# Kernel tuning notes

Measured on AMD Instinct MI355X. Metric: run time of the kernel, lower is better.

The kernel has to match this reference:

```python
import jax, jax.numpy as jnp
import numpy as np

B, H, W, C = 8, 64, 64, 256
NB = 1000  # nms_topn proposals per image


def setup_inputs() -> dict:
    key = jax.random.key(0)
    k1, k2 = jax.random.split(key)
    fm = jax.random.normal(k1, (B, H, W, C), dtype=jnp.float32)
    # normalized boxes [y1,x1,y2,x2] with y1<=y2, x1<=x2
    pts = jax.random.uniform(k2, (B, NB, 2, 2), dtype=jnp.float32)
    pts = jnp.sort(pts, axis=2)  # [B,NB,2(min/max),2(y,x)]
    boxes = jnp.stack([pts[..., 0, 0], pts[..., 0, 1], pts[..., 1, 0], pts[..., 1, 1]], axis=-1)
    return {"feature_map": fm, "roi_bboxes": boxes, "pool_size": 7}


def _crop_and_resize(fm, boxes, box_idx, P):
    """Faithful TF tf.image.crop_and_resize (bilinear, extrapolation_value=0).
    fm: [B,H,W,C]; boxes: [N,4] normalized [y1,x1,y2,x2]; box_idx: [N] int.
    Returns [N,P,P,C]."""
    h, w = fm.shape[1], fm.shape[2]
    y1, x1, y2, x2 = boxes[:, 0], boxes[:, 1], boxes[:, 2], boxes[:, 3]
    t = jnp.arange(P, dtype=fm.dtype)
    # TF sampling grid for crop_size > 1: endpoints inclusive in pixel space
    ys = y1[:, None] * (h - 1) + t * ((y2 - y1)[:, None] * (h - 1) / (P - 1))  # [N,P]
    xs = x1[:, None] * (w - 1) + t * ((x2 - x1)[:, None] * (w - 1) / (P - 1))  # [N,P]

    def lin(coords, size):
        lo = jnp.floor(coords)
        frac = coords - lo
        lo_i = jnp.clip(lo, 0, size - 1).astype(jnp.int32)
        hi_i = jnp.clip(lo + 1, 0, size - 1).astype(jnp.int32)
        valid = (coords >= 0) & (coords <= size - 1)
        return lo_i, hi_i, frac, valid

    y_lo, y_hi, wy, vy = lin(ys, h)
    x_lo, x_hi, wx, vx = lin(xs, w)

    b = box_idx[:, None, None]
    v00 = fm[b, y_lo[:, :, None], x_lo[:, None, :]]  # [N,P,P,C]
    v01 = fm[b, y_lo[:, :, None], x_hi[:, None, :]]
    v10 = fm[b, y_hi[:, :, None], x_lo[:, None, :]]
    v11 = fm[b, y_hi[:, :, None], x_hi[:, None, :]]

    wy_ = wy[:, :, None, None]
    wx_ = wx[:, None, :, None]
    top = v00 + (v01 - v00) * wx_
    bot = v10 + (v11 - v10) * wx_
    out = top + (bot - top) * wy_

    valid = (vy[:, :, None] & vx[:, None, :])[..., None]
    return jnp.where(valid, out, jnp.zeros((), dtype=fm.dtype))


def reference(feature_map, roi_bboxes, pool_size):
    bs, nb = roi_bboxes.shape[0], roi_bboxes.shape[1]
    boxes = roi_bboxes.reshape(bs * nb, 4)
    box_idx = jnp.repeat(jnp.arange(bs, dtype=jnp.int32), nb)
    out = _crop_and_resize(feature_map, boxes, box_idx, pool_size)
    return out.reshape(bs, nb, pool_size, pool_size, feature_map.shape[-1])
```

## Files before the change

### kernel.cpp

```cpp
#include <hip/hip_runtime.h>


#define BATCH 8
#define FH 64
#define FW 64
#define FC 256
#define NBOX 1000
#define PP 7
#define POS_PER_BATCH (NBOX * PP * PP)
#define ROWS_PER_BATCH (NBOX * PP)

typedef __attribute__((ext_vector_type(4))) float f32x4;

__global__ __launch_bounds__(256, 3) void roi_align_kernel(
    const float* __restrict__ fm,
    const float* __restrict__ boxes,
    float* __restrict__ out)
{
    const int lane = threadIdx.x & 63;
    const int wib  = threadIdx.x >> 6;

    const int b    = blockIdx.x & 7;
    const int lblk = blockIdx.x >> 3;
    const int row  = lblk * 4 + wib;

    const int n  = row / PP;
    const int py = row % PP;

    const int c4 = lane * 4;
    const float* __restrict__ fmb = fm + (size_t)b * FH * FW * FC + c4;

    const float* bx = boxes + (b * NBOX + n) * 4;
    const float y1 = bx[0];
    const float x1 = bx[1];
    const float y2 = bx[2];
    const float x2 = bx[3];

    const float yc = y1 * (float)(FH - 1)
                   + (float)py * ((y2 - y1) * (float)(FH - 1) / (float)(PP - 1));
    const float ylo_f = floorf(yc);
    const float wy    = yc - ylo_f;
    int y_lo = (int)ylo_f;
    int y_hi = y_lo + 1;
    y_lo = min(max(y_lo, 0), FH - 1);
    y_hi = min(max(y_hi, 0), FH - 1);
    const bool vy = (yc >= 0.0f) && (yc <= (float)(FH - 1));

    const float xstep = (x2 - x1) * (float)(FW - 1) / (float)(PP - 1);
    const float xbase = x1 * (float)(FW - 1);

    const float* rlo = fmb + (size_t)(y_lo * FW) * FC;
    const float* rhi = fmb + (size_t)(y_hi * FW) * FC;

    float wxv[PP], vmask[PP];
    float4 v00[PP], v01[PP], v10[PP], v11[PP];

    #pragma unroll
    for (int px = 0; px < PP; ++px) {
        const float xc = xbase + (float)px * xstep;
        const float xlo_f = floorf(xc);
        wxv[px] = xc - xlo_f;
        int x_lo = (int)xlo_f;
        int x_hi = x_lo + 1;
        x_lo = min(max(x_lo, 0), FW - 1);
        x_hi = min(max(x_hi, 0), FW - 1);
        const bool vx = (xc >= 0.0f) && (xc <= (float)(FW - 1));
        vmask[px] = (vy && vx) ? 1.0f : 0.0f;

        v00[px] = *(const float4*)(rlo + (size_t)x_lo * FC);
        v01[px] = *(const float4*)(rlo + (size_t)x_hi * FC);
        v10[px] = *(const float4*)(rhi + (size_t)x_lo * FC);
        v11[px] = *(const float4*)(rhi + (size_t)x_hi * FC);
    }

    float* po = out + ((size_t)b * POS_PER_BATCH + (size_t)row * PP) * FC + c4;
    #pragma unroll
    for (int px = 0; px < PP; ++px) {
        const float wx = wxv[px], vm = vmask[px];
        float4 top, bot;
        f32x4 r;
        top.x = v00[px].x + (v01[px].x - v00[px].x) * wx;
        top.y = v00[px].y + (v01[px].y - v00[px].y) * wx;
        top.z = v00[px].z + (v01[px].z - v00[px].z) * wx;
        top.w = v00[px].w + (v01[px].w - v00[px].w) * wx;
        bot.x = v10[px].x + (v11[px].x - v10[px].x) * wx;
        bot.y = v10[px].y + (v11[px].y - v10[px].y) * wx;
        bot.z = v10[px].z + (v11[px].z - v10[px].z) * wx;
        bot.w = v10[px].w + (v11[px].w - v10[px].w) * wx;
        r.x = (top.x + (bot.x - top.x) * wy) * vm;
        r.y = (top.y + (bot.y - top.y) * wy) * vm;
        r.z = (top.z + (bot.z - top.z) * wy) * vm;
        r.w = (top.w + (bot.w - top.w) * wy) * vm;

        __builtin_nontemporal_store(r, (f32x4*)(po + (size_t)px * FC));
    }
}

extern "C" void kernel_launch(void* const* d_in, const int* in_sizes, int n_in,
                              void* d_out, int out_size, void* d_ws, size_t ws_size,
                              hipStream_t stream) {
    const float* fm    = (const float*)d_in[0];
    const float* boxes = (const float*)d_in[1];
    float* out = (float*)d_out;

    const int threads = 256;
    const int blocks  = BATCH * (ROWS_PER_BATCH / 4);

    roi_align_kernel<<<blocks, threads, 0, stream>>>(fm, boxes, out);
}
```

Measured before the change: 81.78 us.

## Convert feature map to bf16 in workspace before bilinear gather

Adds a pre-pass kernel that converts the fp32 feature map to bf16 in the workspace. The ROI-align kernel then gathers bf16 corners, halving gather bytes, and does the interpolation in fp32. The cost is an extra full read and write of the feature map each call, plus rounding error in the output. An fp32 fallback remains for when the workspace is too small.

```diff
diff --git a/kernel.cpp b/kernel.cpp
--- a/kernel.cpp
+++ b/kernel.cpp
@@ -9,11 +9,37 @@
 #define PP 7
 #define POS_PER_BATCH (NBOX * PP * PP)
 #define ROWS_PER_BATCH (NBOX * PP)
+#define FM_ELEMS (BATCH * FH * FW * FC)
 
 typedef __attribute__((ext_vector_type(4))) float f32x4;
 
-__global__ __launch_bounds__(256, 3) void roi_align_kernel(
-    const float* __restrict__ fm,
+__device__ __forceinline__ float bf2f(unsigned short u) {
+    union { unsigned int i; float f; } c;
+    c.i = ((unsigned int)u) << 16;
+    return c.f;
+}
+
+__device__ __forceinline__ unsigned short f2bf(float x) {
+    unsigned int b = __float_as_uint(x);
+    b = (b + 0x7fffu + ((b >> 16) & 1u)) >> 16;
+    return (unsigned short)b;
+}
+
+__global__ __launch_bounds__(256) void fm_convert_kernel(
+    const float4* __restrict__ in, ushort4* __restrict__ out, int n4)
+{
+    int i = blockIdx.x * blockDim.x + threadIdx.x;
+    const int stride = gridDim.x * blockDim.x;
+    for (; i < n4; i += stride) {
+        const float4 v = in[i];
+        ushort4 o;
+        o.x = f2bf(v.x); o.y = f2bf(v.y); o.z = f2bf(v.z); o.w = f2bf(v.w);
+        out[i] = o;
+    }
+}
+
+__global__ __launch_bounds__(256, 4) void roi_align_bf16_kernel(
+    const ushort* __restrict__ fmb16,
     const float* __restrict__ boxes,
     float* __restrict__ out)
 {
@@ -28,7 +54,7 @@
     const int py = row % PP;
 
     const int c4 = lane * 4;
-    const float* __restrict__ fmb = fm + (size_t)b * FH * FW * FC + c4;
+    const ushort* __restrict__ fmb = fmb16 + (size_t)b * FH * FW * FC + c4;
 
     const float* bx = boxes + (b * NBOX + n) * 4;
     const float y1 = bx[0];
@@ -49,11 +75,11 @@
     const float xstep = (x2 - x1) * (float)(FW - 1) / (float)(PP - 1);
     const float xbase = x1 * (float)(FW - 1);
 
-    const float* rlo = fmb + (size_t)(y_lo * FW) * FC;
-    const float* rhi = fmb + (size_t)(y_hi * FW) * FC;
+    const ushort* rlo = fmb + (size_t)(y_lo * FW) * FC;
+    const ushort* rhi = fmb + (size_t)(y_hi * FW) * FC;
 
     float wxv[PP], vmask[PP];
-    float4 v00[PP], v01[PP], v10[PP], v11[PP];
+    ushort4 v00[PP], v01[PP], v10[PP], v11[PP];
 
     #pragma unroll
     for (int px = 0; px < PP; ++px) {
@@ -67,12 +93,95 @@
         const bool vx = (xc >= 0.0f) && (xc <= (float)(FW - 1));
         vmask[px] = (vy && vx) ? 1.0f : 0.0f;
 
+        v00[px] = *(const ushort4*)(rlo + (size_t)x_lo * FC);
+        v01[px] = *(const ushort4*)(rlo + (size_t)x_hi * FC);
+        v10[px] = *(const ushort4*)(rhi + (size_t)x_lo * FC);
+        v11[px] = *(const ushort4*)(rhi + (size_t)x_hi * FC);
+    }
+
+    float* po = out + ((size_t)b * POS_PER_BATCH + (size_t)row * PP) * FC + c4;
+    #pragma unroll
+    for (int px = 0; px < PP; ++px) {
+        const float wx = wxv[px], vm = vmask[px];
+        const float a00x = bf2f(v00[px].x), a01x = bf2f(v01[px].x);
+        const float a00y = bf2f(v00[px].y), a01y = bf2f(v01[px].y);
+        const float a00z = bf2f(v00[px].z), a01z = bf2f(v01[px].z);
+        const float a00w = bf2f(v00[px].w), a01w = bf2f(v01[px].w);
+        const float a10x = bf2f(v10[px].x), a11x = bf2f(v11[px].x);
+        const float a10y = bf2f(v10[px].y), a11y = bf2f(v11[px].y);
+        const float a10z = bf2f(v10[px].z), a11z = bf2f(v11[px].z);
+        const float a10w = bf2f(v10[px].w), a11w = bf2f(v11[px].w);
+
+        float4 top, bot;
+        f32x4 r;
+        top.x = a00x + (a01x - a00x) * wx;
+        top.y = a00y + (a01y - a00y) * wx;
+        top.z = a00z + (a01z - a00z) * wx;
+        top.w = a00w + (a01w - a00w) * wx;
+        bot.x = a10x + (a11x - a10x) * wx;
+        bot.y = a10y + (a11y - a10y) * wx;
+        bot.z = a10z + (a11z - a10z) * wx;
+        bot.w = a10w + (a11w - a10w) * wx;
+        r.x = (top.x + (bot.x - top.x) * wy) * vm;
+        r.y = (top.y + (bot.y - top.y) * wy) * vm;
+        r.z = (top.z + (bot.z - top.z) * wy) * vm;
+        r.w = (top.w + (bot.w - top.w) * wy) * vm;
+
+        __builtin_nontemporal_store(r, (f32x4*)(po + (size_t)px * FC));
+    }
+}
+
+__global__ __launch_bounds__(256, 3) void roi_align_f32_kernel(
+    const float* __restrict__ fm,
+    const float* __restrict__ boxes,
+    float* __restrict__ out)
+{
+    const int lane = threadIdx.x & 63;
+    const int wib  = threadIdx.x >> 6;
+    const int b    = blockIdx.x & 7;
+    const int lblk = blockIdx.x >> 3;
+    const int row  = lblk * 4 + wib;
+    const int n  = row / PP;
+    const int py = row % PP;
+    const int c4 = lane * 4;
+    const float* __restrict__ fmb = fm + (size_t)b * FH * FW * FC + c4;
+
+    const float* bx = boxes + (b * NBOX + n) * 4;
+    const float y1 = bx[0], x1 = bx[1], y2 = bx[2], x2 = bx[3];
+
+    const float yc = y1 * (float)(FH - 1)
+                   + (float)py * ((y2 - y1) * (float)(FH - 1) / (float)(PP - 1));
+    const float ylo_f = floorf(yc);
+    const float wy    = yc - ylo_f;
+    int y_lo = (int)ylo_f;
+    int y_hi = y_lo + 1;
+    y_lo = min(max(y_lo, 0), FH - 1);
+    y_hi = min(max(y_hi, 0), FH - 1);
+    const bool vy = (yc >= 0.0f) && (yc <= (float)(FH - 1));
+
+    const float xstep = (x2 - x1) * (float)(FW - 1) / (float)(PP - 1);
+    const float xbase = x1 * (float)(FW - 1);
+    const float* rlo = fmb + (size_t)(y_lo * FW) * FC;
+    const float* rhi = fmb + (size_t)(y_hi * FW) * FC;
+
+    float wxv[PP], vmask[PP];
+    float4 v00[PP], v01[PP], v10[PP], v11[PP];
+    #pragma unroll
+    for (int px = 0; px < PP; ++px) {
+        const float xc = xbase + (float)px * xstep;
+        const float xlo_f = floorf(xc);
+        wxv[px] = xc - xlo_f;
+        int x_lo = (int)xlo_f;
+        int x_hi = x_lo + 1;
+        x_lo = min(max(x_lo, 0), FW - 1);
+        x_hi = min(max(x_hi, 0), FW - 1);
+        const bool vx = (xc >= 0.0f) && (xc <= (float)(FW - 1));
+        vmask[px] = (vy && vx) ? 1.0f : 0.0f;
         v00[px] = *(const float4*)(rlo + (size_t)x_lo * FC);
         v01[px] = *(const float4*)(rlo + (size_t)x_hi * FC);
         v10[px] = *(const float4*)(rhi + (size_t)x_lo * FC);
         v11[px] = *(const float4*)(rhi + (size_t)x_hi * FC);
     }
-
     float* po = out + ((size_t)b * POS_PER_BATCH + (size_t)row * PP) * FC + c4;
     #pragma unroll
     for (int px = 0; px < PP; ++px) {
@@ -91,7 +200,6 @@
         r.y = (top.y + (bot.y - top.y) * wy) * vm;
         r.z = (top.z + (bot.z - top.z) * wy) * vm;
         r.w = (top.w + (bot.w - top.w) * wy) * vm;
-
         __builtin_nontemporal_store(r, (f32x4*)(po + (size_t)px * FC));
     }
 }
@@ -106,5 +214,13 @@
     const int threads = 256;
     const int blocks  = BATCH * (ROWS_PER_BATCH / 4);
 
-    roi_align_kernel<<<blocks, threads, 0, stream>>>(fm, boxes, out);
-}
+    const size_t need = (size_t)FM_ELEMS * sizeof(unsigned short);
+    if (ws_size >= need) {
+        ushort* fmb16 = (ushort*)d_ws;
+        fm_convert_kernel<<<2048, threads, 0, stream>>>(
+            (const float4*)fm, (ushort4*)fmb16, FM_ELEMS / 4);
+        roi_align_bf16_kernel<<<blocks, threads, 0, stream>>>(fmb16, boxes, out);
+    } else {
+        roi_align_f32_kernel<<<blocks, threads, 0, stream>>>(fm, boxes, out);
+    }
+}
```

Result: slower. 83.52 us (+2.1%).

## Software-pipeline ROI bilinear gathers with two-slot buffer and raise occupancy

Applied to the files above, without the earlier changes.

Replaces the load-all-28-vectors-then-compute structure with a two-stage pipeline: it loads the four corner vectors for pixel px while computing and storing pixel px-1, with sched_barriers fixing the order. This cuts live registers from 28 float4s to 8, and launch bounds move from 3 to 5 blocks per CU to use the freed registers for more resident waves. The catch is that each wave now has fewer loads in flight, since the barriers force it to wait on each pixel's loads before computing. Latency hiding would then rest on extra waves rather than deep memory-level parallelism within a wave.

```diff
diff --git a/kernel.cpp b/kernel.cpp
--- a/kernel.cpp
+++ b/kernel.cpp
@@ -12,7 +12,7 @@
 
 typedef __attribute__((ext_vector_type(4))) float f32x4;
 
-__global__ __launch_bounds__(256, 3) void roi_align_kernel(
+__global__ __launch_bounds__(256, 5) void roi_align_kernel(
     const float* __restrict__ fm,
     const float* __restrict__ boxes,
     float* __restrict__ out)
@@ -52,47 +52,87 @@
     const float* rlo = fmb + (size_t)(y_lo * FW) * FC;
     const float* rhi = fmb + (size_t)(y_hi * FW) * FC;
 
-    float wxv[PP], vmask[PP];
-    float4 v00[PP], v01[PP], v10[PP], v11[PP];
+    float* po = out + ((size_t)b * POS_PER_BATCH + (size_t)row * PP) * FC + c4;
 
-    #pragma unroll
-    for (int px = 0; px < PP; ++px) {
-        const float xc = xbase + (float)px * xstep;
+    float4 t00[2], t01[2], t10[2], t11[2];
+    float  twx[2], tvm[2];
+
+    {
+        const float xc = xbase;
         const float xlo_f = floorf(xc);
-        wxv[px] = xc - xlo_f;
+        twx[0] = xc - xlo_f;
         int x_lo = (int)xlo_f;
         int x_hi = x_lo + 1;
         x_lo = min(max(x_lo, 0), FW - 1);
         x_hi = min(max(x_hi, 0), FW - 1);
         const bool vx = (xc >= 0.0f) && (xc <= (float)(FW - 1));
-        vmask[px] = (vy && vx) ? 1.0f : 0.0f;
-
-        v00[px] = *(const float4*)(rlo + (size_t)x_lo * FC);
-        v01[px] = *(const float4*)(rlo + (size_t)x_hi * FC);
-        v10[px] = *(const float4*)(rhi + (size_t)x_lo * FC);
-        v11[px] = *(const float4*)(rhi + (size_t)x_hi * FC);
+        tvm[0] = (vy && vx) ? 1.0f : 0.0f;
+        t00[0] = *(const float4*)(rlo + (size_t)x_lo * FC);
+        t01[0] = *(const float4*)(rlo + (size_t)x_hi * FC);
+        t10[0] = *(const float4*)(rhi + (size_t)x_lo * FC);
+        t11[0] = *(const float4*)(rhi + (size_t)x_hi * FC);
     }
 
-    float* po = out + ((size_t)b * POS_PER_BATCH + (size_t)row * PP) * FC + c4;
     #pragma unroll
-    for (int px = 0; px < PP; ++px) {
-        const float wx = wxv[px], vm = vmask[px];
+    for (int px = 1; px < PP; ++px) {
+        const int cur = px & 1;
+        const int prv = cur ^ 1;
+
+        const float xc = xbase + (float)px * xstep;
+        const float xlo_f = floorf(xc);
+        twx[cur] = xc - xlo_f;
+        int x_lo = (int)xlo_f;
+        int x_hi = x_lo + 1;
+        x_lo = min(max(x_lo, 0), FW - 1);
+        x_hi = min(max(x_hi, 0), FW - 1);
+        const bool vx = (xc >= 0.0f) && (xc <= (float)(FW - 1));
+        tvm[cur] = (vy && vx) ? 1.0f : 0.0f;
+        t00[cur] = *(const float4*)(rlo + (size_t)x_lo * FC);
+        t01[cur] = *(const float4*)(rlo + (size_t)x_hi * FC);
+        t10[cur] = *(const float4*)(rhi + (size_t)x_lo * FC);
+        t11[cur] = *(const float4*)(rhi + (size_t)x_hi * FC);
+
+        __builtin_amdgcn_sched_barrier(0);
+
+        {
+            const float wx = twx[prv], vm = tvm[prv];
+            float4 top, bot;
+            f32x4 r;
+            top.x = t00[prv].x + (t01[prv].x - t00[prv].x) * wx;
+            top.y = t00[prv].y + (t01[prv].y - t00[prv].y) * wx;
+            top.z = t00[prv].z + (t01[prv].z - t00[prv].z) * wx;
+            top.w = t00[prv].w + (t01[prv].w - t00[prv].w) * wx;
+            bot.x = t10[prv].x + (t11[prv].x - t10[prv].x) * wx;
+            bot.y = t10[prv].y + (t11[prv].y - t10[prv].y) * wx;
+            bot.z = t10[prv].z + (t11[prv].z - t10[prv].z) * wx;
+            bot.w = t10[prv].w + (t11[prv].w - t10[prv].w) * wx;
+            r.x = (top.x + (bot.x - top.x) * wy) * vm;
+            r.y = (top.y + (bot.y - top.y) * wy) * vm;
+            r.z = (top.z + (bot.z - top.z) * wy) * vm;
+            r.w = (top.w + (bot.w - top.w) * wy) * vm;
+            __builtin_nontemporal_store(r, (f32x4*)(po + (size_t)(px - 1) * FC));
+        }
+        __builtin_amdgcn_sched_barrier(0);
+    }
+
+    {
+        const int prv = (PP - 1) & 1;
+        const float wx = twx[prv], vm = tvm[prv];
         float4 top, bot;
         f32x4 r;
-        top.x = v00[px].x + (v01[px].x - v00[px].x) * wx;
-        top.y = v00[px].y + (v01[px].y - v00[px].y) * wx;
-        top.z = v00[px].z + (v01[px].z - v00[px].z) * wx;
-        top.w = v00[px].w + (v01[px].w - v00[px].w) * wx;
-        bot.x = v10[px].x + (v11[px].x - v10[px].x) * wx;
-        bot.y = v10[px].y + (v11[px].y - v10[px].y) * wx;
-        bot.z = v10[px].z + (v11[px].z - v10[px].z) * wx;
-        bot.w = v10[px].w + (v11[px].w - v10[px].w) * wx;
+        top.x = t00[prv].x + (t01[prv].x - t00[prv].x) * wx;
+        top.y = t00[prv].y + (t01[prv].y - t00[prv].y) * wx;
+        top.z = t00[prv].z + (t01[prv].z - t00[prv].z) * wx;
+        top.w = t00[prv].w + (t01[prv].w - t00[prv].w) * wx;
+        bot.x = t10[prv].x + (t11[prv].x - t10[prv].x) * wx;
+        bot.y = t10[prv].y + (t11[prv].y - t10[prv].y) * wx;
+        bot.z = t10[prv].z + (t11[prv].z - t10[prv].z) * wx;
+        bot.w = t10[prv].w + (t11[prv].w - t10[prv].w) * wx;
         r.x = (top.x + (bot.x - top.x) * wy) * vm;
         r.y = (top.y + (bot.y - top.y) * wy) * vm;
         r.z = (top.z + (bot.z - top.z) * wy) * vm;
         r.w = (top.w + (bot.w - top.w) * wy) * vm;
-
-        __builtin_nontemporal_store(r, (f32x4*)(po + (size_t)px * FC));
+        __builtin_nontemporal_store(r, (f32x4*)(po + (size_t)(PP - 1) * FC));
     }
 }
 
```

After: 82.34 us. About the same (+0.7%).
